# Performance work log

Hardware: AMD Instinct MI355X
Metric: run time of the kernel (lower is better)

## Reference

```python
import jax, jax.numpy as jnp
import numpy as np

B, N, C, H = 4, 1024, 1024, 16
D = C // H  # head_dim = 64


def setup_inputs() -> dict:
    key = jax.random.key(0)
    k1, k2, k3 = jax.random.split(key, 3)
    x = jax.random.normal(k1, (B, N, C), dtype=jnp.float32)
    Wqkv = jax.random.normal(k2, (3 * C, C), dtype=jnp.float32) * (C ** -0.5)
    Wproj = jax.random.normal(k3, (C, C), dtype=jnp.float32) * (C ** -0.5)
    bproj = jnp.zeros((C,), dtype=jnp.float32)
    epoch = 25  # selects mask_2 (window w=8) per the original branching
    return {"x": x, "Wqkv": Wqkv, "Wproj": Wproj, "bproj": bproj, "epoch": epoch}


def _band_mask(n, w):
    # get_attn_mask(N, w) == (|i - j| <= w) for every row (boundary cases included)
    idx = jnp.arange(n)
    return jnp.abs(idx[:, None] - idx[None, :]) <= w


def reference(x, Wqkv, Wproj, bproj, epoch):
    b, n, c = x.shape
    d = c // H
    # qkv linear (no bias), then the module's per-head interleaved split:
    # view(B,N,H,3d) -> permute(B,H,N,3d) -> tensor_split into q,k,v
    qkv = jnp.einsum('bnc,oc->bno', x, Wqkv)            # [B,N,3C]
    qkv = qkv.reshape(b, n, H, 3 * d).transpose(0, 2, 1, 3)  # [B,H,N,3d]
    q, k, v = jnp.split(qkv, 3, axis=-1)                # each [B,H,N,d]
    scale = d ** -0.5
    score = jnp.einsum('bhid,bhjd->bhij', q, k) * scale  # [B,H,N,N]
    if epoch is not None and epoch < 50:
        if epoch < 20:
            w = 6
        elif epoch < 30:
            w = 8
        elif epoch < 40:
            w = 10
        else:
            w = 12
        mask = _band_mask(n, w)  # [N,N] bool
        score = jnp.where(mask[None, None], score, jnp.float32(-1e9))
    attn = jax.nn.softmax(score, axis=-1)
    ctx = jnp.einsum('bhij,bhjd->bhid', attn, v)         # [B,H,N,d]
    ctx = ctx.transpose(0, 2, 1, 3).reshape(b, n, c)     # [B,N,C]
    out = jnp.einsum('bnc,oc->bno', ctx, Wproj) + bproj
    return out
```

## Files before the change

kernel.cpp:

```cpp
#include <hip/hip_runtime.h>
#include <hip/hip_bf16.h>


typedef __bf16 bf16x8_t __attribute__((ext_vector_type(8)));
typedef unsigned short u16x8_t __attribute__((ext_vector_type(8)));
typedef float f32x4_t __attribute__((ext_vector_type(4)));

__device__ __forceinline__ void load_lds16(const void* g, void* l) {
    __builtin_amdgcn_global_load_lds(
        (__attribute__((address_space(1))) void*)(g),
        (__attribute__((address_space(3))) void*)(l),
        16, 0, 0);
}

__device__ __forceinline__ u16x8_t cvt8(float4 u, float4 v) {
    union { u16x8_t p; __hip_bfloat16 h[8]; } w;
    w.h[0] = __float2bfloat16(u.x); w.h[1] = __float2bfloat16(u.y);
    w.h[2] = __float2bfloat16(u.z); w.h[3] = __float2bfloat16(u.w);
    w.h[4] = __float2bfloat16(v.x); w.h[5] = __float2bfloat16(v.y);
    w.h[6] = __float2bfloat16(v.z); w.h[7] = __float2bfloat16(v.w);
    return w.p;
}

__global__ __launch_bounds__(512, 2) void gemm1_qkv(
    const float* __restrict__ A,
    const float* __restrict__ B,
    __hip_bfloat16* __restrict__ C)
{
    __shared__ __align__(16) char smem[114688];
    const int tid = threadIdx.x;

    const int orig = blockIdx.y * 16 + blockIdx.x;
    const int xcd = orig & 7, slot = orig >> 3;
    const int hi = slot >> 4;
    const int s  = xcd * 2 + hi;
    const int w  = slot & 15;
    const int m0 = ((s & 3) * 4 + (w & 3)) * 256;
    const int n0 = ((s >> 2) * 4 + (w >> 2)) * 192;

    const int wave = tid >> 6, lane = tid & 63;
    const int wr = wave >> 2, wc = wave & 3;
    const int lr = lane & 15, kg = lane >> 4;
    const int K = 1024, Nn = 3072;

    const int qa0 = tid, qa1 = tid + 512;
    const int qb0 = tid, qb1 = tid + 256;
    const int ra0 = qa0 >> 2, ca0 = ((qa0 & 3) ^ ((ra0 >> 1) & 3)) * 8;
    const int ra1 = qa1 >> 2, ca1 = ((qa1 & 3) ^ ((ra1 >> 1) & 3)) * 8;
    const int rb0 = qb0 >> 2, cb0 = ((qb0 & 3) ^ ((rb0 >> 1) & 3)) * 8;
    const int rb1 = qb1 >> 2, cb1 = ((qb1 & 3) ^ ((rb1 >> 1) & 3)) * 8;
    const float* Ap0 = A + (size_t)(m0 + ra0) * K + ca0;
    const float* Ap1 = A + (size_t)(m0 + ra1) * K + ca1;
    const float* Bp0 = B + (size_t)(n0 + rb0) * K + cb0;
    const float* Bp1 = B + (size_t)(n0 + rb1) * K + cb1;
    const bool bextra = (tid >= 256);

    float4 a00_0 = {}, a01_0 = {}, a10_0 = {}, a11_0 = {};
    float4 b00_0 = {}, b01_0 = {}, b10_0 = {}, b11_0 = {};
    float4 a00_1 = {}, a01_1 = {}, a10_1 = {}, a11_1 = {};
    float4 b00_1 = {}, b01_1 = {}, b10_1 = {}, b11_1 = {};

#define LOADR(S, t) { const int ko_ = (t) * 32;                                  \
    a00_##S = *(const float4*)(Ap0 + ko_); a01_##S = *(const float4*)(Ap0 + ko_ + 4); \
    a10_##S = *(const float4*)(Ap1 + ko_); a11_##S = *(const float4*)(Ap1 + ko_ + 4); \
    b00_##S = *(const float4*)(Bp0 + ko_); b01_##S = *(const float4*)(Bp0 + ko_ + 4); \
    if (bextra) { b10_##S = *(const float4*)(Bp1 + ko_);                         \
                  b11_##S = *(const float4*)(Bp1 + ko_ + 4); } }
#define WRITE(S, t) { char* d_ = smem + ((t) & 3) * 28672;                       \
    *(u16x8_t*)(d_ + qa0 * 16) = cvt8(a00_##S, a01_##S);                         \
    *(u16x8_t*)(d_ + qa1 * 16) = cvt8(a10_##S, a11_##S);                         \
    *(u16x8_t*)(d_ + 16384 + qb0 * 16) = cvt8(b00_##S, b01_##S);                 \
    if (bextra) *(u16x8_t*)(d_ + 16384 + qb1 * 16) = cvt8(b10_##S, b11_##S); }

    f32x4_t acc[8][3] = {};
    const int rsw = ((kg ^ ((lr >> 1) & 3)) * 16);
    const int arow = wr * 128 + lr;
    const int brow = wc * 48 + lr;

#define BODY(S, tval) {                                                          \
    const int t_ = (tval);                                                       \
    const int sb_ = (t_ & 3) * 28672;                                            \
    bf16x8_t a_[8], b_[3];                                                       \
    _Pragma("unroll") for (int mi = 0; mi < 8; ++mi)                             \
        a_[mi] = *(const bf16x8_t*)(smem + sb_ + (arow + mi * 16) * 64 + rsw);   \
    _Pragma("unroll") for (int ni = 0; ni < 3; ++ni)                             \
        b_[ni] = *(const bf16x8_t*)(smem + sb_ + 16384 + (brow + ni * 16) * 64 + rsw); \
    if (t_ < 30) WRITE(S, t_ + 2);                                               \
    if (t_ < 28) LOADR(S, t_ + 4);                                               \
    __builtin_amdgcn_s_setprio(1);                                               \
    _Pragma("unroll") for (int mi = 0; mi < 8; ++mi)                             \
    _Pragma("unroll") for (int ni = 0; ni < 3; ++ni)                             \
        acc[mi][ni] = __builtin_amdgcn_mfma_f32_16x16x32_bf16(                   \
            a_[mi], b_[ni], acc[mi][ni], 0, 0, 0);                               \
    __builtin_amdgcn_s_setprio(0);                                               \
    __syncthreads(); }

    LOADR(0, 0); LOADR(1, 1);
    WRITE(0, 0); WRITE(1, 1);
    LOADR(0, 2); LOADR(1, 3);
    __syncthreads();

    for (int tt = 0; tt < 16; ++tt) {
        BODY(0, tt * 2);
        BODY(1, tt * 2 + 1);
    }
#undef LOADR
#undef WRITE
#undef BODY

    __hip_bfloat16* cl = (__hip_bfloat16*)smem;
#pragma unroll
    for (int mi = 0; mi < 8; ++mi)
#pragma unroll
        for (int ni = 0; ni < 3; ++ni)
#pragma unroll
            for (int r = 0; r < 4; ++r)
                cl[(wr * 128 + mi * 16 + kg * 4 + r) * 200 + wc * 48 + ni * 16 + lr] =
                    __float2bfloat16(acc[mi][ni][r]);
    __syncthreads();
#pragma unroll
    for (int c = 0; c < 12; ++c) {
        const int id = tid + c * 512;
        const int row = id / 24, cc = id - row * 24;
        f32x4_t v = *(const f32x4_t*)(smem + row * 400 + cc * 16);
        *(f32x4_t*)((char*)C + ((size_t)(m0 + row) * Nn + n0) * 2 + cc * 16) = v;
    }
}

__global__ __launch_bounds__(512, 2) void gemm2_proj(
    const __hip_bfloat16* __restrict__ A,
    const float* __restrict__ B,
    float* __restrict__ C,
    const float* __restrict__ bias)
{
    __shared__ __align__(16) char smem[65536];
    const int tid = threadIdx.x;
    const int orig = blockIdx.y * 8 + blockIdx.x;
    const int wgid = (orig & 7) * 32 + (orig >> 3);
    const int m0 = (wgid >> 3) * 128, n0 = (wgid & 7) * 128;

    const int wave = tid >> 6, lane = tid & 63;
    const int wr = wave >> 2, wc = wave & 3;
    const int lr = lane & 15, kg = lane >> 4;
    const int K = 1024, Nn = 1024;

    const int q = tid;
    const int row = q >> 2, cw = ((q & 3) ^ ((row >> 1) & 3)) * 8;
    const __hip_bfloat16* Ap = A + (size_t)(m0 + row) * K + cw;
    const float*          Bp = B + (size_t)(n0 + row) * K + cw;

    float4 av_0 = {}, bva_0 = {}, bvb_0 = {};
    float4 av_1 = {}, bva_1 = {}, bvb_1 = {};

#define LOADR2(S, t) { const int ko_ = (t) * 32;                                 \
    av_##S  = *(const float4*)(Ap + ko_);                      \
    bva_##S = *(const float4*)(Bp + ko_); bvb_##S = *(const float4*)(Bp + ko_ + 4); }
#define WRITE2(S, t) { char* d_ = smem + ((t) & 3) * 16384;                      \
    *(float4*)(d_ + q * 16) = av_##S;                                            \
    *(u16x8_t*)(d_ + 8192 + q * 16) = cvt8(bva_##S, bvb_##S); }

    f32x4_t acc[4][2] = {};
    const int rsw = ((kg ^ ((lr >> 1) & 3)) * 16);
    const int arow = wr * 64 + lr;
    const int brow = wc * 32 + lr;

#define BODY2(S, tval) {                                                         \
    const int t_ = (tval);                                                       \
    const int sb_ = (t_ & 3) * 16384;                                            \
    bf16x8_t a_[4], b_[2];                                                       \
    _Pragma("unroll") for (int mi = 0; mi < 4; ++mi)                             \
        a_[mi] = *(const bf16x8_t*)(smem + sb_ + (arow + mi * 16) * 64 + rsw);   \
    _Pragma("unroll") for (int ni = 0; ni < 2; ++ni)                             \
        b_[ni] = *(const bf16x8_t*)(smem + sb_ + 8192 + (brow + ni * 16) * 64 + rsw); \
    if (t_ < 30) WRITE2(S, t_ + 2);                                              \
    if (t_ < 28) LOADR2(S, t_ + 4);                                              \
    __builtin_amdgcn_s_setprio(1);                                               \
    _Pragma("unroll") for (int mi = 0; mi < 4; ++mi)                             \
    _Pragma("unroll") for (int ni = 0; ni < 2; ++ni)                             \
        acc[mi][ni] = __builtin_amdgcn_mfma_f32_16x16x32_bf16(                   \
            a_[mi], b_[ni], acc[mi][ni], 0, 0, 0);                               \
    __builtin_amdgcn_s_setprio(0);                                               \
    __syncthreads(); }

    LOADR2(0, 0); LOADR2(1, 1);
    WRITE2(0, 0); WRITE2(1, 1);
    LOADR2(0, 2); LOADR2(1, 3);
    __syncthreads();

    for (int tt = 0; tt < 16; ++tt) {
        BODY2(0, tt * 2);
        BODY2(1, tt * 2 + 1);
    }
#undef LOADR2
#undef WRITE2
#undef BODY2

    float* cf = (float*)smem;
#pragma unroll
    for (int p = 0; p < 2; ++p) {
        if (p) __syncthreads();
        if (wr == p) {
#pragma unroll
            for (int mi = 0; mi < 4; ++mi)
#pragma unroll
                for (int ni = 0; ni < 2; ++ni) {
                    const int scol = wc * 32 + ni * 16 + lr;
#pragma unroll
                    for (int r = 0; r < 4; ++r)
                        cf[(mi * 16 + kg * 4 + r) * 132 + scol] = acc[mi][ni][r];
                }
        }
        __syncthreads();
#pragma unroll
        for (int cc = 0; cc < 4; ++cc) {
            const int chunk = tid + cc * 512;
            const int srow = chunk >> 5;
            const int sc = (chunk & 31) * 4;
            f32x4_t v = *(const f32x4_t*)(smem + srow * 528 + sc * 4);
            const f32x4_t bv = *(const f32x4_t*)(bias + n0 + sc);
            v += bv;
            *(f32x4_t*)(C + (size_t)(m0 + p * 64 + srow) * Nn + n0 + sc) = v;
        }
    }
}

__global__ __launch_bounds__(256) void attn_band_mfma(
    const __hip_bfloat16* __restrict__ qkv,
    __hip_bfloat16* __restrict__ ctx,
    const int* __restrict__ epoch_ptr)
{
    __shared__ __align__(16) __hip_bfloat16 K_lds[128 * 64];
    __shared__ __align__(16) __hip_bfloat16 V_lds[64 * 136];
    __shared__ __hip_bfloat16 P_lds[4][16 * 40];

    const int tid = threadIdx.x;
    const int wave = tid >> 6, lane = tid & 63;
    const int lr = lane & 15, kg = lane >> 4;

    const int bid = blockIdx.x;
    const int tg = bid & 15;
    const int bh = bid >> 4;
    const int h = bh & 15, b = bh >> 4;
    const int base = tg * 64;
    const int i0 = base + wave * 16;

    const int e = *epoch_ptr;
    int w;
    if      (e < 20) w = 6;
    else if (e < 30) w = 8;
    else if (e < 40) w = 10;
    else if (e < 50) w = 12;
    else             w = 1023;

    const size_t rowb = (size_t)b * 1024;
    const int hq = h * 192;

#pragma unroll
    for (int it = 0; it < 4; ++it) {
        const int q = tid + it * 256;
        const int row = q >> 3, s = q & 7;
        const int c = s ^ (row & 7);
        int gk = base - 32 + row;
        gk = gk < 0 ? 0 : (gk > 1023 ? 1023 : gk);
        load_lds16(qkv + (rowb + gk) * 3072 + hq + 64 + c * 8,
                   (char*)K_lds + q * 16);
    }
    {
        const int pr = tid & 63, dg = tid >> 6;
        int gk0 = base - 32 + 2 * pr, gk1 = gk0 + 1;
        gk0 = gk0 < 0 ? 0 : (gk0 > 1023 ? 1023 : gk0);
        gk1 = gk1 < 0 ? 0 : (gk1 > 1023 ? 1023 : gk1);
        const __hip_bfloat16* v0 = qkv + (rowb + gk0) * 3072 + hq + 128 + dg * 16;
        const __hip_bfloat16* v1 = qkv + (rowb + gk1) * 3072 + hq + 128 + dg * 16;
        u16x8_t a0 = *(const u16x8_t*)v0, b0 = *(const u16x8_t*)(v0 + 8);
        u16x8_t a1 = *(const u16x8_t*)v1, b1 = *(const u16x8_t*)(v1 + 8);
#pragma unroll
        for (int c2 = 0; c2 < 8; ++c2) {
            *(unsigned int*)&V_lds[(dg * 16 + c2) * 136 + 2 * pr] =
                (unsigned int)a0[c2] | ((unsigned int)a1[c2] << 16);
            *(unsigned int*)&V_lds[(dg * 16 + 8 + c2) * 136 + 2 * pr] =
                (unsigned int)b0[c2] | ((unsigned int)b1[c2] << 16);
        }
    }

    bf16x8_t aq[2];
#pragma unroll
    for (int ks = 0; ks < 2; ++ks)
        aq[ks] = *(const bf16x8_t*)(qkv + (rowb + i0 + lr) * 3072 + hq + ks * 32 + kg * 8);

    __syncthreads();

    float m[4] = {-1e30f, -1e30f, -1e30f, -1e30f};
    float l[4] = {0.f, 0.f, 0.f, 0.f};
    f32x4_t o[4] = {};

    int jlo = i0 - w;      if (jlo < 0) jlo = 0;
    int jhi = i0 + 15 + w; if (jhi > 1023) jhi = 1023;
    const int t0 = (base >> 5) - 1;

    for (int p = (jlo >> 5); p <= (jhi >> 5); ++p) {
        const int kb = p * 32;
        const int tl = p - t0;

        f32x4_t s2[2] = {};
#pragma unroll
        for (int t = 0; t < 2; ++t)
#pragma unroll
            for (int ks = 0; ks < 2; ++ks) {
                const int lkr = tl * 32 + t * 16 + lr;
                bf16x8_t bk = *(const bf16x8_t*)(
                    (char*)K_lds + lkr * 128 + (((ks * 4 + kg) ^ (lr & 7)) * 16));
                s2[t] = __builtin_amdgcn_mfma_f32_16x16x32_bf16(aq[ks], bk, s2[t], 0, 0, 0);
            }

        float sv[2][4];
#pragma unroll
        for (int t = 0; t < 2; ++t)
#pragma unroll
            for (int r = 0; r < 4; ++r) {
                const int qi = i0 + kg * 4 + r;
                const int j  = kb + t * 16 + lr;
                int d = qi - j; if (d < 0) d = -d;
                sv[t][r] = (d <= w) ? s2[t][r] * 0.125f : -1e30f;
            }

        float tm[4];
#pragma unroll
        for (int r = 0; r < 4; ++r) tm[r] = fmaxf(sv[0][r], sv[1][r]);
#pragma unroll
        for (int msk = 1; msk < 16; msk <<= 1)
#pragma unroll
            for (int r = 0; r < 4; ++r) tm[r] = fmaxf(tm[r], __shfl_xor(tm[r], msk));

        float sc[4], ps[4], pvv[2][4];
#pragma unroll
        for (int r = 0; r < 4; ++r) {
            const float mn = fmaxf(m[r], tm[r]);
            sc[r] = __expf(m[r] - mn);
            pvv[0][r] = __expf(sv[0][r] - mn);
            pvv[1][r] = __expf(sv[1][r] - mn);
            ps[r] = pvv[0][r] + pvv[1][r];
            m[r] = mn;
        }
#pragma unroll
        for (int msk = 1; msk < 16; msk <<= 1)
#pragma unroll
            for (int r = 0; r < 4; ++r) ps[r] += __shfl_xor(ps[r], msk);
#pragma unroll
        for (int r = 0; r < 4; ++r) l[r] = l[r] * sc[r] + ps[r];
#pragma unroll
        for (int ni = 0; ni < 4; ++ni)
#pragma unroll
            for (int r = 0; r < 4; ++r) o[ni][r] *= sc[r];

#pragma unroll
        for (int t = 0; t < 2; ++t)
#pragma unroll
            for (int r = 0; r < 4; ++r)
                P_lds[wave][(kg * 4 + r) * 40 + t * 16 + lr] =
                    __float2bfloat16(pvv[t][r]);

        bf16x8_t ap = *(const bf16x8_t*)&P_lds[wave][lr * 40 + kg * 8];
#pragma unroll
        for (int ni = 0; ni < 4; ++ni) {
            bf16x8_t bv = *(const bf16x8_t*)&V_lds[(ni * 16 + lr) * 136 + tl * 32 + kg * 8];
            o[ni] = __builtin_amdgcn_mfma_f32_16x16x32_bf16(ap, bv, o[ni], 0, 0, 0);
        }
    }

#pragma unroll
    for (int ni = 0; ni < 4; ++ni)
#pragma unroll
        for (int r = 0; r < 4; ++r)
            ctx[(rowb + i0 + kg * 4 + r) * 1024 + h * 64 + ni * 16 + lr] =
                __float2bfloat16(o[ni][r] / l[r]);
}

extern "C" void kernel_launch(void* const* d_in, const int* in_sizes, int n_in,
                              void* d_out, int out_size, void* d_ws, size_t ws_size,
                              hipStream_t stream)
{
    const float* x     = (const float*)d_in[0];
    const float* Wqkv  = (const float*)d_in[1];
    const float* Wproj = (const float*)d_in[2];
    const float* bproj = (const float*)d_in[3];
    const int*   epoch = (const int*)d_in[4];

    char* ws = (char*)d_ws;
    __hip_bfloat16* qkvb = (__hip_bfloat16*)(ws);
    __hip_bfloat16* ctxb = (__hip_bfloat16*)(ws + 25165824);

    gemm1_qkv<<<dim3(16, 16), 512, 0, stream>>>(x, Wqkv, qkvb);

    attn_band_mfma<<<1024, 256, 0, stream>>>(qkvb, ctxb, epoch);

    gemm2_proj<<<dim3(8, 32), 512, 0, stream>>>(
        ctxb, Wproj, (float*)d_out, bproj);
}
```

Baseline: 68.05 us.

## Halve QKV GEMM M-tile to 128 and use double-buffered LDS for occupancy

Shrinks the QKV projection GEMM tile from 256x192 to 128x192 and doubles the grid to 512 workgroups. The LDS ring goes from four stages to two, cutting shared memory from 112KB to 40KB, and launch bounds allow 4 blocks per CU. The epilogue is staged in two halves through the smaller LDS. This trades per-block data reuse and pipeline depth for more workgroups and higher occupancy, which should improve load balance across CUs. The XCD-aware tile swizzle is redone for the new grid.

```diff
diff --git a/kernel.cpp b/kernel.cpp
--- a/kernel.cpp
+++ b/kernel.cpp
@@ -22,108 +22,104 @@
     return w.p;
 }
 
-__global__ __launch_bounds__(512, 2) void gemm1_qkv(
+__global__ __launch_bounds__(512, 4) void gemm1_qkv(
     const float* __restrict__ A,
     const float* __restrict__ B,
     __hip_bfloat16* __restrict__ C)
 {
-    __shared__ __align__(16) char smem[114688];
+    __shared__ __align__(16) char smem[40960];
     const int tid = threadIdx.x;
 
     const int orig = blockIdx.y * 16 + blockIdx.x;
-    const int xcd = orig & 7, slot = orig >> 3;
-    const int hi = slot >> 4;
-    const int s  = xcd * 2 + hi;
-    const int w  = slot & 15;
-    const int m0 = ((s & 3) * 4 + (w & 3)) * 256;
-    const int n0 = ((s >> 2) * 4 + (w >> 2)) * 192;
+    const int xcd = orig & 7, rest = orig >> 3;
+    const int s  = xcd * 4 + (rest >> 4);
+    const int lo = rest & 15;
+    const int m0 = ((s & 7) * 4 + (lo & 3)) * 128;
+    const int n0 = ((s >> 3) * 4 + (lo >> 2)) * 192;
 
     const int wave = tid >> 6, lane = tid & 63;
     const int wr = wave >> 2, wc = wave & 3;
     const int lr = lane & 15, kg = lane >> 4;
     const int K = 1024, Nn = 3072;
 
-    const int qa0 = tid, qa1 = tid + 512;
-    const int qb0 = tid, qb1 = tid + 256;
-    const int ra0 = qa0 >> 2, ca0 = ((qa0 & 3) ^ ((ra0 >> 1) & 3)) * 8;
-    const int ra1 = qa1 >> 2, ca1 = ((qa1 & 3) ^ ((ra1 >> 1) & 3)) * 8;
+    const int qa = tid, qb0 = tid, qb1 = tid + 512;
+    const int ra  = qa  >> 2, ca  = ((qa  & 3) ^ ((ra  >> 1) & 3)) * 8;
     const int rb0 = qb0 >> 2, cb0 = ((qb0 & 3) ^ ((rb0 >> 1) & 3)) * 8;
     const int rb1 = qb1 >> 2, cb1 = ((qb1 & 3) ^ ((rb1 >> 1) & 3)) * 8;
-    const float* Ap0 = A + (size_t)(m0 + ra0) * K + ca0;
-    const float* Ap1 = A + (size_t)(m0 + ra1) * K + ca1;
+    const float* Ap  = A + (size_t)(m0 + ra)  * K + ca;
     const float* Bp0 = B + (size_t)(n0 + rb0) * K + cb0;
     const float* Bp1 = B + (size_t)(n0 + rb1) * K + cb1;
-    const bool bextra = (tid >= 256);
-
-    float4 a00_0 = {}, a01_0 = {}, a10_0 = {}, a11_0 = {};
-    float4 b00_0 = {}, b01_0 = {}, b10_0 = {}, b11_0 = {};
-    float4 a00_1 = {}, a01_1 = {}, a10_1 = {}, a11_1 = {};
-    float4 b00_1 = {}, b01_1 = {}, b10_1 = {}, b11_1 = {};
-
-#define LOADR(S, t) { const int ko_ = (t) * 32;                                  \
-    a00_##S = *(const float4*)(Ap0 + ko_); a01_##S = *(const float4*)(Ap0 + ko_ + 4); \
-    a10_##S = *(const float4*)(Ap1 + ko_); a11_##S = *(const float4*)(Ap1 + ko_ + 4); \
-    b00_##S = *(const float4*)(Bp0 + ko_); b01_##S = *(const float4*)(Bp0 + ko_ + 4); \
-    if (bextra) { b10_##S = *(const float4*)(Bp1 + ko_);                         \
-                  b11_##S = *(const float4*)(Bp1 + ko_ + 4); } }
-#define WRITE(S, t) { char* d_ = smem + ((t) & 3) * 28672;                       \
-    *(u16x8_t*)(d_ + qa0 * 16) = cvt8(a00_##S, a01_##S);                         \
-    *(u16x8_t*)(d_ + qa1 * 16) = cvt8(a10_##S, a11_##S);                         \
-    *(u16x8_t*)(d_ + 16384 + qb0 * 16) = cvt8(b00_##S, b01_##S);                 \
-    if (bextra) *(u16x8_t*)(d_ + 16384 + qb1 * 16) = cvt8(b10_##S, b11_##S); }
-
-    f32x4_t acc[8][3] = {};
+    const bool bextra = (tid < 256);
+
+    float4 av0 = {}, av1 = {};
+    float4 b0a = {}, b0b = {}, b1a = {}, b1b = {};
+
+#define LOADR(t) { const int ko_ = (t) * 32;                                    \
+    av0 = *(const float4*)(Ap + ko_);  av1 = *(const float4*)(Ap + ko_ + 4);    \
+    b0a = *(const float4*)(Bp0 + ko_); b0b = *(const float4*)(Bp0 + ko_ + 4);   \
+    if (bextra) { b1a = *(const float4*)(Bp1 + ko_);                            \
+                  b1b = *(const float4*)(Bp1 + ko_ + 4); } }
+#define WRITE(t) { char* d_ = smem + ((t) & 1) * 20480;                         \
+    *(u16x8_t*)(d_ + qa * 16) = cvt8(av0, av1);                                 \
+    *(u16x8_t*)(d_ + 8192 + qb0 * 16) = cvt8(b0a, b0b);                         \
+    if (bextra) *(u16x8_t*)(d_ + 8192 + qb1 * 16) = cvt8(b1a, b1b); }
+
+    f32x4_t acc[4][3] = {};
     const int rsw = ((kg ^ ((lr >> 1) & 3)) * 16);
-    const int arow = wr * 128 + lr;
+    const int arow = wr * 64 + lr;
     const int brow = wc * 48 + lr;
 
-#define BODY(S, tval) {                                                          \
-    const int t_ = (tval);                                                       \
-    const int sb_ = (t_ & 3) * 28672;                                            \
-    bf16x8_t a_[8], b_[3];                                                       \
-    _Pragma("unroll") for (int mi = 0; mi < 8; ++mi)                             \
-        a_[mi] = *(const bf16x8_t*)(smem + sb_ + (arow + mi * 16) * 64 + rsw);   \
-    _Pragma("unroll") for (int ni = 0; ni < 3; ++ni)                             \
-        b_[ni] = *(const bf16x8_t*)(smem + sb_ + 16384 + (brow + ni * 16) * 64 + rsw); \
-    if (t_ < 30) WRITE(S, t_ + 2);                                               \
-    if (t_ < 28) LOADR(S, t_ + 4);                                               \
-    __builtin_amdgcn_s_setprio(1);                                               \
-    _Pragma("unroll") for (int mi = 0; mi < 8; ++mi)                             \
-    _Pragma("unroll") for (int ni = 0; ni < 3; ++ni)                             \
-        acc[mi][ni] = __builtin_amdgcn_mfma_f32_16x16x32_bf16(                   \
-            a_[mi], b_[ni], acc[mi][ni], 0, 0, 0);                               \
-    __builtin_amdgcn_s_setprio(0);                                               \
-    __syncthreads(); }
-
-    LOADR(0, 0); LOADR(1, 1);
-    WRITE(0, 0); WRITE(1, 1);
-    LOADR(0, 2); LOADR(1, 3);
+    LOADR(0); WRITE(0);
+    LOADR(1);
     __syncthreads();
 
-    for (int tt = 0; tt < 16; ++tt) {
-        BODY(0, tt * 2);
-        BODY(1, tt * 2 + 1);
+    for (int t = 0; t < 32; ++t) {
+        const int sb_ = (t & 1) * 20480;
+        bf16x8_t a_[4], b_[3];
+#pragma unroll
+        for (int mi = 0; mi < 4; ++mi)
+            a_[mi] = *(const bf16x8_t*)(smem + sb_ + (arow + mi * 16) * 64 + rsw);
+#pragma unroll
+        for (int ni = 0; ni < 3; ++ni)
+            b_[ni] = *(const bf16x8_t*)(smem + sb_ + 8192 + (brow + ni * 16) * 64 + rsw);
+        if (t < 31) WRITE(t + 1);
+        if (t < 30) LOADR(t + 2);
+        __builtin_amdgcn_s_setprio(1);
+#pragma unroll
+        for (int mi = 0; mi < 4; ++mi)
+#pragma unroll
+            for (int ni = 0; ni < 3; ++ni)
+                acc[mi][ni] = __builtin_amdgcn_mfma_f32_16x16x32_bf16(
+                    a_[mi], b_[ni], acc[mi][ni], 0, 0, 0);
+        __builtin_amdgcn_s_setprio(0);
+        __syncthreads();
     }
 #undef LOADR
 #undef WRITE
-#undef BODY
 
     __hip_bfloat16* cl = (__hip_bfloat16*)smem;
 #pragma unroll
-    for (int mi = 0; mi < 8; ++mi)
-#pragma unroll
-        for (int ni = 0; ni < 3; ++ni)
-#pragma unroll
-            for (int r = 0; r < 4; ++r)
-                cl[(wr * 128 + mi * 16 + kg * 4 + r) * 200 + wc * 48 + ni * 16 + lr] =
-                    __float2bfloat16(acc[mi][ni][r]);
-    __syncthreads();
-#pragma unroll
-    for (int c = 0; c < 12; ++c) {
-        const int id = tid + c * 512;
-        const int row = id / 24, cc = id - row * 24;
-        f32x4_t v = *(const f32x4_t*)(smem + row * 400 + cc * 16);
-        *(f32x4_t*)((char*)C + ((size_t)(m0 + row) * Nn + n0) * 2 + cc * 16) = v;
+    for (int p = 0; p < 2; ++p) {
+        if (p) __syncthreads();
+        if (wr == p) {
+#pragma unroll
+            for (int mi = 0; mi < 4; ++mi)
+#pragma unroll
+                for (int ni = 0; ni < 3; ++ni)
+#pragma unroll
+                    for (int r = 0; r < 4; ++r)
+                        cl[(mi * 16 + kg * 4 + r) * 200 + wc * 48 + ni * 16 + lr] =
+                            __float2bfloat16(acc[mi][ni][r]);
+        }
+        __syncthreads();
+#pragma unroll
+        for (int c = 0; c < 3; ++c) {
+            const int id = tid + c * 512;
+            const int row = id / 24, cc = id - row * 24;
+            f32x4_t v = *(const f32x4_t*)(smem + row * 400 + cc * 16);
+            *(f32x4_t*)((char*)C + ((size_t)(m0 + p * 64 + row) * Nn + n0) * 2 +
+                        cc * 16) = v;
+        }
     }
 }
 
@@ -390,7 +386,7 @@
     __hip_bfloat16* qkvb = (__hip_bfloat16*)(ws);
     __hip_bfloat16* ctxb = (__hip_bfloat16*)(ws + 25165824);
 
-    gemm1_qkv<<<dim3(16, 16), 512, 0, stream>>>(x, Wqkv, qkvb);
+    gemm1_qkv<<<dim3(16, 32), 512, 0, stream>>>(x, Wqkv, qkvb);
 
     attn_band_mfma<<<1024, 256, 0, stream>>>(qkvb, ctxb, epoch);
 
```

New measurement: 70.26 us. 3.2% more time.
